# Performance work log

Hardware: AMD Instinct MI355X
Metric: run time of the kernel (lower is better)

Reference implementation:

```python
import jax, jax.numpy as jnp
import numpy as np

B, N, DE = 8, 1024, 128
R, DR = 8, 64
D = DE + DR


def setup_inputs() -> dict:
    key = jax.random.key(0)
    k1, k2, k3 = jax.random.split(key, 3)
    node_encodings = jax.random.normal(k1, (B, N, DE), dtype=jnp.float32)
    relation_encodings = jax.random.normal(k2, (B, R, DR), dtype=jnp.float32)
    # xavier_uniform over (R, D): bound = sqrt(6 / (R + D))
    bound = np.sqrt(6.0 / (R + D)).astype(np.float32)
    relations_weights_bilinear = jax.random.uniform(
        k3, (R, D), dtype=jnp.float32, minval=-bound, maxval=bound)
    return {
        "node_encodings": node_encodings,
        "relation_encodings": relation_encodings,
        "relations_weights_bilinear": relations_weights_bilinear,
    }


def reference(node_encodings, relation_encodings, relations_weights_bilinear):
    # node_encodings: [B, N, De]; relation_encodings: [B, R, Dr]; weights: [R, De+Dr]
    b, n, de = node_encodings.shape
    r, dr = relation_encodings.shape[1], relation_encodings.shape[2]
    nodes = jnp.broadcast_to(node_encodings[:, None, :, :], (b, r, n, de))
    rels = jnp.broadcast_to(relation_encodings[:, :, None, :], (b, r, n, dr))
    er = jnp.concatenate([nodes, rels], axis=-1)  # [B, R, N, D]
    # diag(w) matmul == elementwise scale along feature dim
    scaled = er * relations_weights_bilinear[None, :, None, :]  # [B, R, N, D]
    scores = jnp.einsum('brnd,brmd->brnm', scaled, er)  # [B, R, N, N]
    return jax.nn.sigmoid(scores)
```

## Files before the change

### kernel.cpp

```cpp
#include <hip/hip_runtime.h>
#include <hip/hip_bf16.h>


typedef __attribute__((ext_vector_type(8))) short bf16x8;
typedef __attribute__((ext_vector_type(4))) float f32x4;

constexpr int Bc = 8, Nc = 1024, DEc = 128, Rc = 8, DRc = 64, Dc = 192;
constexpr int TILE = 128;

static __device__ __forceinline__ unsigned short f2bf(float x) {
    __hip_bfloat16 h = __float2bfloat16(x);
    return *reinterpret_cast<unsigned short*>(&h);
}

static __device__ __forceinline__ float fast_sigmoid(float x) {
    float e;
    asm("v_exp_f32 %0, %1" : "=v"(e) : "v"(x * -1.44269504f));
    float s;
    asm("v_rcp_f32 %0, %1" : "=v"(s) : "v"(e + 1.0f));
    return s;
}

__global__ __launch_bounds__(512, 4) void rdm6(
    const float* __restrict__ node,
    const float* __restrict__ rel,
    const float* __restrict__ w,
    float* __restrict__ out)
{
    __shared__ float smem[17408];
    unsigned short* As = (unsigned short*)smem;
    unsigned short* Bs = (unsigned short*)smem + 16384;

    const int lin = blockIdx.x;
    const int b   = lin & 7;
    const int r   = (lin >> 3) & 7;
    const int t   = lin >> 6;
    const int ntile = t >> 3;
    const int mtile = t & 7;
    const int n0 = ntile * TILE;
    const int m0 = mtile * TILE;

    const int tid  = threadIdx.x;
    const int lane = tid & 63;
    const int wid  = tid >> 6;

    const float* wrp   = w + r * Dc;
    const float* relbr = rel + ((long)b * Rc + r) * DRc;

    float cv = wrp[DEc + lane] * relbr[lane] * relbr[lane];
    #pragma unroll
    for (int o = 32; o > 0; o >>= 1) cv += __shfl_xor(cv, o, 64);
    const float c = cv;

    const float* nodeb = node + (long)b * Nc * DEc;
    const int col4 = (tid & 31) * 4;
    const int row0 = tid >> 5;
    const float4 wv4 = *(const float4*)(wrp + col4);

    #pragma unroll
    for (int p = 0; p < 8; ++p) {
        const int row = row0 + p * 16;
        const float4 av = *(const float4*)(nodeb + (long)(n0 + row) * DEc + col4);
        const float4 bv = *(const float4*)(nodeb + (long)(m0 + row) * DEc + col4);
        const int e = (row * TILE + col4) ^ ((row & 7) << 3);
        union { ushort4 u4; unsigned short h[4]; } pa, pb;
        pa.h[0] = f2bf(av.x * wv4.x);
        pa.h[1] = f2bf(av.y * wv4.y);
        pa.h[2] = f2bf(av.z * wv4.z);
        pa.h[3] = f2bf(av.w * wv4.w);
        pb.h[0] = f2bf(bv.x);
        pb.h[1] = f2bf(bv.y);
        pb.h[2] = f2bf(bv.z);
        pb.h[3] = f2bf(bv.w);
        *(ushort4*)&As[e] = pa.u4;
        *(ushort4*)&Bs[e] = pb.u4;
    }
    __syncthreads();

    const int wm0 = (wid >> 2) * 64;
    const int wn0 = (wid & 3) * 32;
    const int lr  = lane & 15;
    const int lk  = (lane >> 4) * 8;

    f32x4 acc[4][2] = {};

    #pragma unroll
    for (int kk = 0; kk < 4; ++kk) {
        bf16x8 afr[4], bfr[2];
        #pragma unroll
        for (int mi = 0; mi < 4; ++mi) {
            const int rowA = wm0 + mi * 16 + lr;
            afr[mi] = *(const bf16x8*)&Bs[(rowA * TILE + kk * 32 + lk) ^ ((rowA & 7) << 3)];
        }
        #pragma unroll
        for (int ni = 0; ni < 2; ++ni) {
            const int rowB = wn0 + ni * 16 + lr;
            bfr[ni] = *(const bf16x8*)&As[(rowB * TILE + kk * 32 + lk) ^ ((rowB & 7) << 3)];
        }
        #pragma unroll
        for (int mi = 0; mi < 4; ++mi)
            #pragma unroll
            for (int ni = 0; ni < 2; ++ni)
                acc[mi][ni] = __builtin_amdgcn_mfma_f32_16x16x32_bf16(
                    afr[mi], bfr[ni], acc[mi][ni], 0, 0, 0);
    }

    __syncthreads();

    float* tb = smem + wid * (32 * 68);

    #pragma unroll
    for (int mi = 0; mi < 4; ++mi) {
        #pragma unroll
        for (int ni = 0; ni < 2; ++ni) {
            const int n_t = ni * 16 + lr;
            const int m_t = mi * 16 + (lane >> 4) * 4;
            f32x4 v;
            v[0] = fast_sigmoid(acc[mi][ni][0] + c);
            v[1] = fast_sigmoid(acc[mi][ni][1] + c);
            v[2] = fast_sigmoid(acc[mi][ni][2] + c);
            v[3] = fast_sigmoid(acc[mi][ni][3] + c);
            *(f32x4*)&tb[n_t * 68 + m_t] = v;
        }
    }
    asm volatile("s_waitcnt lgkmcnt(0)" ::: "memory");

    float* outbr = out + (long)(b * Rc + r) * Nc * Nc
                 + (long)(n0 + wn0) * Nc + (m0 + wm0);
    #pragma unroll
    for (int p = 0; p < 8; ++p) {
        const int n_t = p * 4 + (lane >> 4);
        const int m_t = (lane & 15) * 4;
        const f32x4 v = *(const f32x4*)&tb[n_t * 68 + m_t];
        *(f32x4*)(outbr + (long)n_t * Nc + m_t) = v;
    }
}

extern "C" void kernel_launch(void* const* d_in, const int* in_sizes, int n_in,
                              void* d_out, int out_size, void* d_ws, size_t ws_size,
                              hipStream_t stream) {
    const float* node = (const float*)d_in[0];
    const float* rel  = (const float*)d_in[1];
    const float* w    = (const float*)d_in[2];
    float* out = (float*)d_out;

    rdm6<<<Bc * Rc * 64, 512, 0, stream>>>(node, rel, w, out);
}
```

Measured before the change: 63.23 us.

## Exploit score symmetry: compute upper-triangle tiles and write transposed copies

```diff
diff --git a/kernel.cpp b/kernel.cpp
--- a/kernel.cpp
+++ b/kernel.cpp
@@ -21,7 +21,7 @@
     return s;
 }
 
-__global__ __launch_bounds__(512, 4) void rdm6(
+__global__ __launch_bounds__(512, 4) void rdm7(
     const float* __restrict__ node,
     const float* __restrict__ rel,
     const float* __restrict__ w,
@@ -31,14 +31,18 @@
     unsigned short* As = (unsigned short*)smem;
     unsigned short* Bs = (unsigned short*)smem + 16384;
 
-    const int lin = blockIdx.x;
-    const int b   = lin & 7;
-    const int r   = (lin >> 3) & 7;
-    const int t   = lin >> 6;
-    const int ntile = t >> 3;
-    const int mtile = t & 7;
-    const int n0 = ntile * TILE;
-    const int m0 = mtile * TILE;
+    const int lin  = blockIdx.x;
+    const int b    = lin & 7;
+    const int rest = lin >> 3;
+    const int r    = rest & 7;
+    const int tp   = rest >> 3;
+
+    int i = 0, acc0 = 0;
+    while (tp >= acc0 + (8 - i)) { acc0 += 8 - i; ++i; }
+    const int j = i + (tp - acc0);
+    const int n0 = i * TILE;
+    const int m0 = j * TILE;
+    const bool offdiag = (i != j);
 
     const int tid  = threadIdx.x;
     const int lane = tid & 63;
@@ -125,14 +129,32 @@
     }
     asm volatile("s_waitcnt lgkmcnt(0)" ::: "memory");
 
-    float* outbr = out + (long)(b * Rc + r) * Nc * Nc
-                 + (long)(n0 + wn0) * Nc + (m0 + wm0);
-    #pragma unroll
-    for (int p = 0; p < 8; ++p) {
-        const int n_t = p * 4 + (lane >> 4);
-        const int m_t = (lane & 15) * 4;
-        const f32x4 v = *(const f32x4*)&tb[n_t * 68 + m_t];
-        *(f32x4*)(outbr + (long)n_t * Nc + m_t) = v;
+    float* plane = out + (long)(b * Rc + r) * Nc * Nc;
+
+    {
+        float* outd = plane + (long)(n0 + wn0) * Nc + (m0 + wm0);
+        #pragma unroll
+        for (int p = 0; p < 8; ++p) {
+            const int n_t = p * 4 + (lane >> 4);
+            const int m_t = (lane & 15) * 4;
+            const f32x4 v = *(const f32x4*)&tb[n_t * 68 + m_t];
+            *(f32x4*)(outd + (long)n_t * Nc + m_t) = v;
+        }
+    }
+
+    if (offdiag) {
+        float* outt = plane + (long)(m0 + wm0) * Nc + (n0 + wn0);
+        #pragma unroll
+        for (int p = 0; p < 8; ++p) {
+            const int m_t = p * 8 + (lane >> 3);
+            const int n_t = (lane & 7) * 4;
+            f32x4 v;
+            v[0] = tb[(n_t + 0) * 68 + m_t];
+            v[1] = tb[(n_t + 1) * 68 + m_t];
+            v[2] = tb[(n_t + 2) * 68 + m_t];
+            v[3] = tb[(n_t + 3) * 68 + m_t];
+            *(f32x4*)(outt + (long)m_t * Nc + n_t) = v;
+        }
     }
 }
 
@@ -144,5 +166,5 @@
     const float* w    = (const float*)d_in[2];
     float* out = (float*)d_out;
 
-    rdm6<<<Bc * Rc * 64, 512, 0, stream>>>(node, rel, w, out);
+    rdm7<<<Bc * Rc * 36, 512, 0, stream>>>(node, rel, w, out);
 }
```

After: 56.85 us. -10.1%, faster.
